# Optimization experiments

Hardware: AMD Instinct MI355X
Metric: run time of the kernel (lower is better)

The kernel has to match this reference:

```python
import jax, jax.numpy as jnp
import numpy as np

STRIDES = (8, 16, 32, 64, 128)
LEVEL_HW = ((128, 160), (64, 80), (32, 40), (16, 20), (8, 10))
IMG_H, IMG_W = 1024, 1280
B, NUM_CLASSES = 16, 20
SCORE_THR, IOU_THR, MAX_DET = 0.05, 0.6, 1000


def _coords_all():
    # coords_fmap2orig for every level, concatenated -> [N, 2] (x, y)
    cs = []
    for (h, w), s in zip(LEVEL_HW, STRIDES):
        sx = jnp.arange(w, dtype=jnp.float32) * s + s // 2
        sy = jnp.arange(h, dtype=jnp.float32) * s + s // 2
        yy, xx = jnp.meshgrid(sy, sx, indexing='ij')
        cs.append(jnp.stack([xx.reshape(-1), yy.reshape(-1)], -1))
    return jnp.concatenate(cs, 0)


def _reshape_cat(levels):
    # list of [B,C,h,w] -> [B, sum(h*w), C]
    return jnp.concatenate(
        [p.transpose(0, 2, 3, 1).reshape(p.shape[0], -1, p.shape[1]) for p in levels], 1)


def _decode(cls_l, cnt_l, reg_l, coords):
    cls = jax.nn.sigmoid(_reshape_cat(cls_l))           # [B,N,C]
    cnt = jax.nn.sigmoid(_reshape_cat(cnt_l))[..., 0]   # [B,N]
    reg = _reshape_cat(reg_l)                           # [B,N,4] ltrb
    scores = jnp.sqrt(jnp.max(cls, -1) * cnt)           # add_centerness + sqrt
    classes = jnp.argmax(cls, -1) + 1
    boxes = jnp.concatenate([coords[None] - reg[..., :2], coords[None] + reg[..., 2:]], -1)
    return scores, classes, boxes


def _nms_keep(boxes, scores, classes, valid):
    # masked greedy per-class NMS on fixed size M; returns keep mask [M]
    boxes = jax.lax.stop_gradient(boxes)
    scores = jax.lax.stop_gradient(scores)
    maxc = jnp.max(jnp.where(valid[:, None], boxes, 0.0))
    b = boxes + (classes.astype(boxes.dtype) * (maxc + 1.0))[:, None]  # class offsets
    order = jnp.argsort(-jnp.where(valid, scores, -jnp.inf))
    b = b[order]
    v = valid[order]
    x1, y1, x2, y2 = b[:, 0], b[:, 1], b[:, 2], b[:, 3]
    areas = (x2 - x1 + 1.0) * (y2 - y1 + 1.0)
    iw = jnp.clip(jnp.minimum(x2[:, None], x2[None, :]) - jnp.maximum(x1[:, None], x1[None, :]) + 1.0, 0.0)
    ih = jnp.clip(jnp.minimum(y2[:, None], y2[None, :]) - jnp.maximum(y1[:, None], y1[None, :]) + 1.0, 0.0)
    inter = iw * ih
    iou = inter / (areas[:, None] + areas[None, :] - inter)
    M = boxes.shape[0]

    def body(i, carry):
        keep, sup = carry
        k = v[i] & (~sup[i])
        keep = keep.at[i].set(k)
        sup = sup | (k & (iou[i] > IOU_THR))
        return keep, sup

    keep_s, _ = jax.lax.fori_loop(0, M, body, (jnp.zeros(M, bool), jnp.zeros(M, bool)))
    return jnp.zeros(M, bool).at[order].set(keep_s)


def _forward(args):
    cls_r, cnt_r, reg_r = args[0:5], args[5:10], args[10:15]
    cls_i, cnt_i, reg_i = args[15:20], args[20:25], args[25:30]
    coords = _coords_all()
    s_r, c_r, b_r = _decode(cls_r, cnt_r, reg_r, coords)
    s_i, c_i, b_i = _decode(cls_i, cnt_i, reg_i, coords)
    scores = jnp.concatenate([s_r, s_i], 1)   # [B, 2N]
    classes = jnp.concatenate([c_r, c_i], 1)
    boxes = jnp.concatenate([b_r, b_i], 1)
    top_s, top_i = jax.lax.top_k(scores, MAX_DET)
    top_c = jnp.take_along_axis(classes, top_i, 1)
    top_b = jnp.take_along_axis(boxes, top_i[..., None], 1)
    valid = top_s >= SCORE_THR
    keep = jax.vmap(_nms_keep)(top_b, top_s, top_c, valid)
    # ClipBoxes: clamp to image bounds
    top_b = jnp.maximum(top_b, 0.0)
    xs = jnp.minimum(top_b[..., 0::2], IMG_W - 1.0)
    ys = jnp.minimum(top_b[..., 1::2], IMG_H - 1.0)
    top_b = jnp.stack([xs[..., 0], ys[..., 0], xs[..., 1], ys[..., 1]], -1)
    kf = keep.astype(top_s.dtype)
    return top_s * kf, top_c * keep, top_b * kf[..., None], keep


def setup_inputs() -> dict:
    key = jax.random.key(0)
    chans = {'cls': NUM_CLASSES, 'cnt': 1, 'reg': 4}
    inp = {}
    i = 0
    for mod in ('r', 'i'):
        for kind in ('cls', 'cnt', 'reg'):
            for l, (h, w) in enumerate(LEVEL_HW):
                k = jax.random.fold_in(key, i); i += 1
                inp[f'{kind}_{mod}_{l}'] = jax.random.normal(k, (B, chans[kind], h, w), jnp.float32)
    return inp


def reference(cls_r_0, cls_r_1, cls_r_2, cls_r_3, cls_r_4,
              cnt_r_0, cnt_r_1, cnt_r_2, cnt_r_3, cnt_r_4,
              reg_r_0, reg_r_1, reg_r_2, reg_r_3, reg_r_4,
              cls_i_0, cls_i_1, cls_i_2, cls_i_3, cls_i_4,
              cnt_i_0, cnt_i_1, cnt_i_2, cnt_i_3, cnt_i_4,
              reg_i_0, reg_i_1, reg_i_2, reg_i_3, reg_i_4):
    args = [cls_r_0, cls_r_1, cls_r_2, cls_r_3, cls_r_4,
            cnt_r_0, cnt_r_1, cnt_r_2, cnt_r_3, cnt_r_4,
            reg_r_0, reg_r_1, reg_r_2, reg_r_3, reg_r_4,
            cls_i_0, cls_i_1, cls_i_2, cls_i_3, cls_i_4,
            cnt_i_0, cnt_i_1, cnt_i_2, cnt_i_3, cnt_i_4,
            reg_i_0, reg_i_1, reg_i_2, reg_i_3, reg_i_4]
    return _forward(args)
```

## Files before the change

### kernel.cpp

```cpp
#include <hip/hip_runtime.h>
#include <hip/hip_bf16.h>

typedef unsigned long long u64;
typedef unsigned int u32;

#define NTOT    54560
#define NMOD    27280
#define BATCH   16
#define KPAD    1024
#define MAXD    1000
#define NBIN    16384
#define CANDCAP 6144
#define NLDSPOS 25600

struct Ptrs { const float* p[30]; };

constexpr size_t SZ_KEY   = (size_t)BATCH * NTOT * 8;
constexpr size_t SZ_TOPK  = (size_t)BATCH * KPAD * 8;
constexpr size_t SZ_TRAW  = (size_t)BATCH * KPAD * 16;
constexpr size_t SZ_T1    = (size_t)BATCH * KPAD * 4;
constexpr size_t SZ_MAXC  = (size_t)BATCH * 32 * 4;
constexpr size_t SZ_VALID = (size_t)BATCH * 32 * 4;
constexpr size_t SZ_MASK  = (size_t)BATCH * KPAD * 32 * 4;

constexpr size_t OFF_KEY    = 0;
constexpr size_t OFF_TOPK   = OFF_KEY   + SZ_KEY;
constexpr size_t OFF_TRAW   = OFF_TOPK  + SZ_TOPK;
constexpr size_t OFF_TSCORE = OFF_TRAW  + SZ_TRAW;
constexpr size_t OFF_TCLSF  = OFF_TSCORE+ SZ_T1;
constexpr size_t OFF_MAXC   = OFF_TCLSF + SZ_T1;
constexpr size_t OFF_VALID  = OFF_MAXC  + SZ_MAXC;
constexpr size_t OFF_MASK   = OFF_VALID + SZ_VALID;

__device__ inline void level_of(int nm, int& l, int& pos, int& w, int& s, int& hw) {
    if (nm < 20480)      { l = 0; pos = nm;         w = 160; s = 8;   hw = 20480; }
    else if (nm < 25600) { l = 1; pos = nm - 20480; w = 80;  s = 16;  hw = 5120; }
    else if (nm < 26880) { l = 2; pos = nm - 25600; w = 40;  s = 32;  hw = 1280; }
    else if (nm < 27200) { l = 3; pos = nm - 26880; w = 20;  s = 64;  hw = 320; }
    else                 { l = 4; pos = nm - 27200; w = 10;  s = 128; hw = 80; }
}

__device__ inline float sigm(float x) { return 1.0f / (1.0f + expf(-x)); }

__device__ inline void ld_lds16(const float* g, float* l) {
    __builtin_amdgcn_global_load_lds(
        (const __attribute__((address_space(1))) void*)g,
        (__attribute__((address_space(3))) void*)l, 16, 0, 0);
}

__global__ __launch_bounds__(256)
void decode_lds_kernel(Ptrs ptrs, u64* __restrict__ keyAll) {
    __shared__ float lds[21 * 1024];
    int cc = blockIdx.x;
    int b = blockIdx.y;
    int mod = cc / 25, c = cc % 25;
    int l     = (c < 20) ? 0 : 1;
    int hw    = (c < 20) ? 20480 : 5120;
    int pos0  = (c < 20) ? c * 1024 : (c - 20) * 1024;
    int nmb   = (l == 0) ? pos0 : 20480 + pos0;
    const float* clsP = ptrs.p[mod * 15 + l];
    const float* cntP = ptrs.p[mod * 15 + 5 + l];
    int wave = threadIdx.x >> 6, lane = threadIdx.x & 63;

    const float* cbase = clsP + (size_t)b * 20 * hw + pos0 + wave * 256 + lane * 4;
    float* dbase = lds + wave * 256;
    #pragma unroll
    for (int ch = 0; ch < 20; ++ch)
        ld_lds16(cbase + (size_t)ch * hw, dbase + ch * 1024);
    ld_lds16(cntP + (size_t)b * hw + pos0 + wave * 256 + lane * 4, dbase + 20 * 1024);
    __syncthreads();

    int t = threadIdx.x;
    const float4* l4 = (const float4*)lds;
    float4 mx = l4[t];
    #pragma unroll
    for (int ch = 1; ch < 20; ++ch) {
        float4 v = l4[ch * 256 + t];
        mx.x = fmaxf(mx.x, v.x); mx.y = fmaxf(mx.y, v.y);
        mx.z = fmaxf(mx.z, v.z); mx.w = fmaxf(mx.w, v.w);
    }
    float4 cv = l4[20 * 256 + t];

    int n = mod * NMOD + nmb + t * 4;
    u32 s0 = __float_as_uint(sqrtf(__fmul_rn(sigm(mx.x), sigm(cv.x))));
    u32 s1 = __float_as_uint(sqrtf(__fmul_rn(sigm(mx.y), sigm(cv.y))));
    u32 s2 = __float_as_uint(sqrtf(__fmul_rn(sigm(mx.z), sigm(cv.z))));
    u32 s3 = __float_as_uint(sqrtf(__fmul_rn(sigm(mx.w), sigm(cv.w))));
    ulonglong2* ka2 = (ulonglong2*)(keyAll + (size_t)b * NTOT + n);
    ulonglong2 k01, k23;
    k01.x = ((u64)s0 << 16) | (u64)(65535 - n);
    k01.y = ((u64)s1 << 16) | (u64)(65535 - (n + 1));
    k23.x = ((u64)s2 << 16) | (u64)(65535 - (n + 2));
    k23.y = ((u64)s3 << 16) | (u64)(65535 - (n + 3));
    ka2[0] = k01; ka2[1] = k23;
}

__global__ __launch_bounds__(256)
void decode_tail_kernel(Ptrs ptrs, u64* __restrict__ keyAll) {
    int t = blockIdx.x * 256 + threadIdx.x;
    int b = blockIdx.y;
    if (t >= 3360) return;
    int mod = t / 1680;
    int tm = t % 1680;
    int q = t & 3;
    int nm = 25600 + (tm & ~3);
    int l, pos, w, s, hw;
    level_of(nm, l, pos, w, s, hw);
    (void)w; (void)s;
    const float* clsP = ptrs.p[mod * 15 + l];
    const float* cntP = ptrs.p[mod * 15 + 5 + l];
    const float4* cb = (const float4*)(clsP + (size_t)b * 20 * hw + pos);
    int hw4 = hw >> 2;
    int c0 = q * 5;
    float4 v[5];
    #pragma unroll
    for (int c = 0; c < 5; ++c) v[c] = cb[(size_t)(c0 + c) * hw4];
    float4 cv = *(const float4*)(cntP + (size_t)b * hw + pos);

    float4 mx = v[0];
    #pragma unroll
    for (int c = 1; c < 5; ++c) {
        mx.x = fmaxf(mx.x, v[c].x); mx.y = fmaxf(mx.y, v[c].y);
        mx.z = fmaxf(mx.z, v[c].z); mx.w = fmaxf(mx.w, v[c].w);
    }
    mx.x = fmaxf(mx.x, __shfl_xor(mx.x, 1));
    mx.y = fmaxf(mx.y, __shfl_xor(mx.y, 1));
    mx.z = fmaxf(mx.z, __shfl_xor(mx.z, 1));
    mx.w = fmaxf(mx.w, __shfl_xor(mx.w, 1));
    mx.x = fmaxf(mx.x, __shfl_xor(mx.x, 2));
    mx.y = fmaxf(mx.y, __shfl_xor(mx.y, 2));
    mx.z = fmaxf(mx.z, __shfl_xor(mx.z, 2));
    mx.w = fmaxf(mx.w, __shfl_xor(mx.w, 2));

    float ma = (q & 1) ? ((q & 2) ? mx.w : mx.y) : ((q & 2) ? mx.z : mx.x);
    float ca = (q & 1) ? ((q & 2) ? cv.w : cv.y) : ((q & 2) ? cv.z : cv.x);
    u32 sb = __float_as_uint(sqrtf(__fmul_rn(sigm(ma), sigm(ca))));
    int n = mod * NMOD + nm + q;
    keyAll[(size_t)b * NTOT + n] = ((u64)sb << 16) | (u64)(65535 - n);
}

__global__ __launch_bounds__(1024)
void select_kernel(const u64* __restrict__ keyAll, u64* __restrict__ topkey,
                   u32* __restrict__ maxcG) {
    int b = blockIdx.x, tid = threadIdx.x;
    int lane = tid & 63, wid = tid >> 6;
    __shared__ u32 shist[NBIN];
    __shared__ u32 warep[16];
    __shared__ int sB1;
    __shared__ u32 scnt;
    double* sd = (double*)shist;

    if (tid == 0) { maxcG[b * 32] = 0u; scnt = 0u; }
    #pragma unroll
    for (int j = 0; j < NBIN / 1024; ++j) shist[tid + j * 1024] = 0u;
    __syncthreads();

    const u64* keys = keyAll + (size_t)b * NTOT;
    const u64 SENT = ~0ull;
    for (int n0 = 0; n0 < NTOT; n0 += 8192) {
        u64 kk[8];
        #pragma unroll
        for (int r = 0; r < 8; ++r) {
            int idx = n0 + r * 1024 + tid;
            kk[r] = (idx < NTOT) ? keys[idx] : SENT;
        }
        #pragma unroll
        for (int r = 0; r < 8; ++r)
            if (kk[r] != SENT) atomicAdd(&shist[(u32)(kk[r] >> 32)], 1u);
    }
    __syncthreads();

    u32 loc[16]; u32 sum = 0;
    #pragma unroll
    for (int j = 0; j < 16; ++j) { loc[j] = shist[NBIN - 1 - (tid * 16 + j)]; sum += loc[j]; }
    u32 v = sum;
    #pragma unroll
    for (int off = 1; off < 64; off <<= 1) {
        u32 t2 = (u32)__shfl_up((int)v, off);
        if (lane >= off) v += t2;
    }
    if (lane == 63) warep[wid] = v;
    __syncthreads();
    if (tid < 16) {
        u32 p = warep[tid];
        #pragma unroll
        for (int off = 1; off < 16; off <<= 1) {
            u32 t2 = (u32)__shfl_up((int)p, off);
            if (tid >= off) p += t2;
        }
        warep[tid] = p;
    }
    __syncthreads();
    u32 incl = v + (wid ? warep[wid - 1] : 0u);
    u32 excl = incl - sum;
    if (excl < (u32)MAXD && incl >= (u32)MAXD) {
        u32 c = excl;
        #pragma unroll
        for (int j = 0; j < 16; ++j) {
            c += loc[j];
            if (c >= (u32)MAXD) { sB1 = NBIN - 1 - (tid * 16 + j); break; }
        }
    }
    __syncthreads();
    int B1 = sB1;

    for (int n0 = 0; n0 < NTOT; n0 += 8192) {
        u64 kk[8];
        #pragma unroll
        for (int r = 0; r < 8; ++r) {
            int idx = n0 + r * 1024 + tid;
            kk[r] = (idx < NTOT) ? keys[idx] : 0ull;
        }
        #pragma unroll
        for (int r = 0; r < 8; ++r) {
            if (kk[r] != 0ull && (int)(kk[r] >> 32) >= B1) {
                u32 p = atomicAdd(&scnt, 1u);
                if (p < CANDCAP - 2) sd[p] = (double)kk[r];
            }
        }
    }
    __syncthreads();
    int C = min((int)scnt, CANDCAP - 2);
    if (tid == 0) { sd[C] = -1.0; sd[C + 1] = -1.0; }
    __syncthreads();

    for (int i = tid; i < C; i += 1024) {
        double ki = sd[i];
        int rank = 0;
        const double2* sd2 = (const double2*)sd;
        int C2 = (C + 1) >> 1;
        for (int j = 0; j < C2; ++j) {
            double2 v2 = sd2[j];
            rank += (v2.x > ki) ? 1 : 0;
            rank += (v2.y > ki) ? 1 : 0;
        }
        if (rank < MAXD) topkey[(size_t)b * KPAD + rank] = (u64)ki;
    }
}

__global__ __launch_bounds__(128)
void gather_kernel(Ptrs ptrs, const u64* __restrict__ topkey,
                   float4* __restrict__ traw, float* __restrict__ tscore,
                   float* __restrict__ tclsf, u32* __restrict__ validwords,
                   u32* __restrict__ maxcG) {
    #pragma clang fp contract(off)
    int b = blockIdx.y;
    int tid = threadIdx.x;
    int half = tid & 1;
    int i = blockIdx.x * 64 + (tid >> 1);
    int active = (i < MAXD);

    float score = 0.f;
    float best = -1.0f; int bi = 0;
    float ra = 0.f, rb2 = 0.f;
    int pos = 0, w = 1, s = 0;
    if (active) {
        u64 key = topkey[(size_t)b * KPAD + i];
        int n = 65535 - (int)(key & 0xFFFFull);
        score = __uint_as_float((u32)(key >> 16));
        int mod = (n >= NMOD) ? 1 : 0;
        int nm = n - mod * NMOD;
        int l, hw;
        level_of(nm, l, pos, w, s, hw);
        const float* clsP = ptrs.p[mod * 15 + l];
        const float* regP = ptrs.p[mod * 15 + 10 + l];
        const float* cbp = clsP + (size_t)b * 20 * hw + pos;
        const float* rbp = regP + (size_t)b * 4 * hw + pos;
        float cl[10];
        int c0 = half * 10;
        #pragma unroll
        for (int c = 0; c < 10; ++c) cl[c] = cbp[(size_t)(c0 + c) * hw];
        ra  = rbp[(size_t)(half * 2) * hw];
        rb2 = rbp[(size_t)(half * 2 + 1) * hw];
        #pragma unroll
        for (int c = 0; c < 10; ++c) {
            float p = sigm(cl[c]);
            if (p > best) { best = p; bi = c0 + c; }
        }
    }
    float po  = __shfl_xor(best, 1);
    int   bio = __shfl_xor(bi, 1);
    float rao = __shfl_xor(ra, 1);
    float rbo = __shfl_xor(rb2, 1);
    if (half == 0) { if (po > best)  { best = po; bi = bio; } }
    else           { if (po >= best) { best = po; bi = bio; } }
    float clsf = active ? (float)(bi + 1) : 0.f;
    float r0 = half ? rao : ra,  r1 = half ? rbo : rb2;
    float r2 = half ? ra  : rao, r3 = half ? rb2 : rbo;

    float4 bx = make_float4(0.f, 0.f, 0.f, 0.f);
    if (active) {
        int xi = pos % w, yi = pos / w;
        float cx = (float)(xi * s + (s >> 1));
        float cy = (float)(yi * s + (s >> 1));
        bx.x = cx - r0; bx.y = cy - r1; bx.z = cx + r2; bx.w = cy + r3;
    }
    int valid = active && (score >= 0.05f) && (half == 0);
    float contrib = valid ? fmaxf(0.0f, fmaxf(fmaxf(bx.x, bx.y), fmaxf(bx.z, bx.w))) : 0.0f;
    float red = contrib;
    #pragma unroll
    for (int off = 32; off > 0; off >>= 1) red = fmaxf(red, __shfl_down(red, off));
    if ((tid & 63) == 0) atomicMax(&maxcG[b * 32], __float_as_uint(red));
    u64 ball = __ballot(valid != 0);
    if ((tid & 63) == 0) {
        u32 word = 0;
        for (int j = 0; j < 32; ++j) word |= (u32)((ball >> (2 * j)) & 1ull) << j;
        validwords[b * 32 + blockIdx.x * 2 + (tid >> 6)] = word;
    }
    if (half == 0) {
        size_t oo = (size_t)b * KPAD + i;
        traw[oo] = bx; tscore[oo] = score; tclsf[oo] = clsf;
    }
}

#define SW(t) ((((t) & 31) << 3) | ((t) >> 5))
__global__ __launch_bounds__(64)
void mask_kernel(const float4* __restrict__ traw, const float* __restrict__ tclsf,
                 const u32* __restrict__ maxcG, u32* __restrict__ maskG) {
    #pragma clang fp contract(off)
    int u = blockIdx.x, b = blockIdx.y, tid = threadIdx.x;
    int g, wg;
    if (u < 128)      { g = u >> 2;                 wg = u & 3; }
    else if (u < 224) { int i2 = u - 128; g = 32 + i2 / 3;      wg = 1 + i2 % 3; }
    else if (u < 288) { int i2 = u - 224; g = 64 + (i2 >> 1);   wg = 2 + (i2 & 1); }
    else              { g = 96 + (u - 288);         wg = 3; }
    int i0 = g * 8, j0 = wg * 256;
    float m1 = __uint_as_float(maxcG[b * 32]) + 1.0f;

    __shared__ float cx1[256], cy1[256], cx2[256], cy2[256], ca[256];
    for (int t = tid; t < 256; t += 64) {
        float4 f = traw[(size_t)b * KPAD + j0 + t];
        float o = __fmul_rn(tclsf[(size_t)b * KPAD + j0 + t], m1);
        float ox1 = __fadd_rn(f.x, o), oy1 = __fadd_rn(f.y, o);
        float ox2 = __fadd_rn(f.z, o), oy2 = __fadd_rn(f.w, o);
        float dw = ox2 - ox1 + 1.0f;
        float dh = oy2 - oy1 + 1.0f;
        int ts = SW(t);
        cx1[ts] = ox1; cy1[ts] = oy1; cx2[ts] = ox2; cy2[ts] = oy2;
        ca[ts] = __fmul_rn(dw, dh);
    }
    __syncthreads();

    int ir = tid >> 3, wr = tid & 7;
    int i = i0 + ir;
    float4 fi = traw[(size_t)b * KPAD + i];
    float oi = __fmul_rn(tclsf[(size_t)b * KPAD + i], m1);
    float ix1 = __fadd_rn(fi.x, oi), iy1 = __fadd_rn(fi.y, oi);
    float ix2 = __fadd_rn(fi.z, oi), iy2 = __fadd_rn(fi.w, oi);
    float dwi = ix2 - ix1 + 1.0f, dhi = iy2 - iy1 + 1.0f;
    float ai = __fmul_rn(dwi, dhi);
    u32 bits = 0;
    int jb = wr * 32;
    for (int jj = 0; jj < 32; ++jj) {
        int js = SW(jb + jj);
        float iw = fminf(ix2, cx2[js]) - fmaxf(ix1, cx1[js]) + 1.0f;
        iw = fmaxf(iw, 0.0f);
        float ih = fminf(iy2, cy2[js]) - fmaxf(iy1, cy1[js]) + 1.0f;
        ih = fmaxf(ih, 0.0f);
        float inter = iw * ih;
        float denom = (ai + ca[js]) - inter;
        float iou = inter / denom;
        bits |= (iou > 0.6f) ? (1u << jj) : 0u;
    }
    maskG[((size_t)b * KPAD + i) * 32 + wg * 8 + wr] = bits;
}

__global__ __launch_bounds__(512)
void scan_out_kernel(const u32* __restrict__ maskG, const u32* __restrict__ validbits,
                     const float4* __restrict__ traw, const float* __restrict__ tscore,
                     const float* __restrict__ tclsf, float* __restrict__ out) {
    __shared__ u32 sm[KPAD * 32];
    __shared__ u32 keeps[32];
    int b = blockIdx.x, tid = threadIdx.x;

    const uint4* s4 = (const uint4*)(maskG + (size_t)b * KPAD * 32);
    uint4* d4 = (uint4*)sm;
    #pragma unroll
    for (int r = 0; r < 16; ++r) d4[tid + r * 512] = s4[tid + r * 512];
    __syncthreads();

    if (tid < 64) {
        int lane = tid, lw = lane & 31;
        u32 vreg = (lane < 32) ? validbits[b * 32 + lane] : 0u;
        u32 removed = 0u, keepw = 0u;
        u32 mA[8], mB[8];
        #pragma unroll
        for (int d = 0; d < 8; ++d) {
            mA[d] = sm[d * 32 + lw];
            mB[d] = sm[(d + 8) * 32 + lw];
        }
        auto step8 = [&](int base, u32* ms) {
            #pragma unroll
            for (int d = 0; d < 8; ++d) {
                int i = base + d;
                int wi = i >> 5, bi2 = i & 31;
                u32 rw = (u32)__builtin_amdgcn_readlane((int)removed, wi);
                u32 vw = (u32)__builtin_amdgcn_readlane((int)vreg, wi);
                u32 k = ((vw >> bi2) & 1u) & (~(rw >> bi2) & 1u);
                if (k) removed |= ms[d];
                if (lane == wi) keepw |= (k << bi2);
                ms[d] = sm[(i + 16) * 32 + lw];
            }
        };
        for (int t = 0; t < 62; ++t) { step8(t * 16, mA); step8(t * 16 + 8, mB); }
        step8(992, mA);
        if (lane < 32) keeps[lane] = keepw;
    }
    __syncthreads();

    const int BQ = BATCH * MAXD;
    for (int s2 = tid; s2 < MAXD; s2 += 512) {
        u32 kf = (keeps[s2 >> 5] >> (s2 & 31)) & 1u;
        size_t oo = (size_t)b * KPAD + s2;
        float score = tscore[oo];
        float clsf = tclsf[oo];
        float4 bx = traw[oo];
        float x1 = fminf(fmaxf(bx.x, 0.f), 1279.f);
        float y1 = fminf(fmaxf(bx.y, 0.f), 1023.f);
        float x2 = fminf(fmaxf(bx.z, 0.f), 1279.f);
        float y2 = fminf(fmaxf(bx.w, 0.f), 1023.f);
        int base = b * MAXD + s2;
        out[base] = kf ? score : 0.0f;
        out[BQ + base] = kf ? clsf : 0.0f;
        float* ob = out + 2 * BQ + (size_t)base * 4;
        ob[0] = kf ? x1 : 0.f; ob[1] = kf ? y1 : 0.f;
        ob[2] = kf ? x2 : 0.f; ob[3] = kf ? y2 : 0.f;
        out[6 * BQ + base] = kf ? 1.0f : 0.0f;
    }
}

extern "C" void kernel_launch(void* const* d_in, const int* in_sizes, int n_in,
                              void* d_out, int out_size, void* d_ws, size_t ws_size,
                              hipStream_t stream) {
    Ptrs ptrs;
    for (int i = 0; i < 30; ++i) ptrs.p[i] = (const float*)d_in[i];

    char* ws = (char*)d_ws;
    u64*    keyAll    = (u64*)   (ws + OFF_KEY);
    u64*    topkey    = (u64*)   (ws + OFF_TOPK);
    float4* traw      = (float4*)(ws + OFF_TRAW);
    float*  tscore    = (float*) (ws + OFF_TSCORE);
    float*  tclsf     = (float*) (ws + OFF_TCLSF);
    u32*    maxcG     = (u32*)   (ws + OFF_MAXC);
    u32*    validbits = (u32*)   (ws + OFF_VALID);
    u32*    maskG     = (u32*)   (ws + OFF_MASK);
    float*  out       = (float*)d_out;

    decode_lds_kernel<<<dim3(50, BATCH), 256, 0, stream>>>(ptrs, keyAll);
    decode_tail_kernel<<<dim3(14, BATCH), 256, 0, stream>>>(ptrs, keyAll);
    select_kernel<<<BATCH, 1024, 0, stream>>>(keyAll, topkey, maxcG);
    gather_kernel<<<dim3(16, BATCH), 128, 0, stream>>>(ptrs, topkey, traw, tscore, tclsf,
                                                       validbits, maxcG);
    mask_kernel<<<dim3(320, BATCH), 64, 0, stream>>>(traw, tclsf, maxcG, maskG);
    scan_out_kernel<<<BATCH, 512, 0, stream>>>(maskG, validbits, traw, tscore, tclsf, out);
}
```

Measured before the change: 277.6 us.

## Fuse decode kernels, bucket-based top-k ranking, and larger mask tiles

Merges the two decode kernels into one launch with smaller 128-thread blocks. In the select kernel, it replaces the O(C^2) all-pairs rank count over doubles with a counting-sort scatter into histogram-bin buckets, followed by ranking within each bin. It also stages the top-k in LDS before writing it out. The mask kernel is retiled to 256-thread blocks covering 32 rows each, so fewer blocks are launched. The main risk is ranking cost when one bin holds many candidates, and the candidate count being capped at CAND.

Result: faster. 253.2 us (-8.8%).

```diff
diff --git a/kernel.cpp b/kernel.cpp
--- a/kernel.cpp
+++ b/kernel.cpp
@@ -10,8 +10,7 @@
 #define KPAD    1024
 #define MAXD    1000
 #define NBIN    16384
-#define CANDCAP 6144
-#define NLDSPOS 25600
+#define CAND    6144
 
 struct Ptrs { const float* p[30]; };
 
@@ -48,15 +47,57 @@
         (__attribute__((address_space(3))) void*)l, 16, 0, 0);
 }
 
-__global__ __launch_bounds__(256)
-void decode_lds_kernel(Ptrs ptrs, u64* __restrict__ keyAll) {
-    __shared__ float lds[21 * 1024];
+__global__ __launch_bounds__(128)
+void decode_kernel(Ptrs ptrs, u64* __restrict__ keyAll) {
+    __shared__ float lds[21 * 512];
     int cc = blockIdx.x;
     int b = blockIdx.y;
-    int mod = cc / 25, c = cc % 25;
-    int l     = (c < 20) ? 0 : 1;
-    int hw    = (c < 20) ? 20480 : 5120;
-    int pos0  = (c < 20) ? c * 1024 : (c - 20) * 1024;
+
+    if (cc >= 100) {
+        int t = (cc - 100) * 128 + threadIdx.x;
+        if (t >= 3360) return;
+        int mod = t / 1680;
+        int tm = t % 1680;
+        int q = t & 3;
+        int nm = 25600 + (tm & ~3);
+        int l, pos, w, s, hw;
+        level_of(nm, l, pos, w, s, hw);
+        (void)w; (void)s;
+        const float* clsP = ptrs.p[mod * 15 + l];
+        const float* cntP = ptrs.p[mod * 15 + 5 + l];
+        const float4* cb = (const float4*)(clsP + (size_t)b * 20 * hw + pos);
+        int hw4 = hw >> 2;
+        int c0 = q * 5;
+        float4 v[5];
+        #pragma unroll
+        for (int c = 0; c < 5; ++c) v[c] = cb[(size_t)(c0 + c) * hw4];
+        float4 cv = *(const float4*)(cntP + (size_t)b * hw + pos);
+        float4 mx = v[0];
+        #pragma unroll
+        for (int c = 1; c < 5; ++c) {
+            mx.x = fmaxf(mx.x, v[c].x); mx.y = fmaxf(mx.y, v[c].y);
+            mx.z = fmaxf(mx.z, v[c].z); mx.w = fmaxf(mx.w, v[c].w);
+        }
+        mx.x = fmaxf(mx.x, __shfl_xor(mx.x, 1));
+        mx.y = fmaxf(mx.y, __shfl_xor(mx.y, 1));
+        mx.z = fmaxf(mx.z, __shfl_xor(mx.z, 1));
+        mx.w = fmaxf(mx.w, __shfl_xor(mx.w, 1));
+        mx.x = fmaxf(mx.x, __shfl_xor(mx.x, 2));
+        mx.y = fmaxf(mx.y, __shfl_xor(mx.y, 2));
+        mx.z = fmaxf(mx.z, __shfl_xor(mx.z, 2));
+        mx.w = fmaxf(mx.w, __shfl_xor(mx.w, 2));
+        float ma = (q & 1) ? ((q & 2) ? mx.w : mx.y) : ((q & 2) ? mx.z : mx.x);
+        float ca = (q & 1) ? ((q & 2) ? cv.w : cv.y) : ((q & 2) ? cv.z : cv.x);
+        u32 sb = __float_as_uint(sqrtf(__fmul_rn(sigm(ma), sigm(ca))));
+        int n = mod * NMOD + nm + q;
+        keyAll[(size_t)b * NTOT + n] = ((u64)sb << 16) | (u64)(65535 - n);
+        return;
+    }
+
+    int mod = cc / 50, c = cc % 50;
+    int l     = (c < 40) ? 0 : 1;
+    int hw    = (c < 40) ? 20480 : 5120;
+    int pos0  = (c < 40) ? c * 512 : (c - 40) * 512;
     int nmb   = (l == 0) ? pos0 : 20480 + pos0;
     const float* clsP = ptrs.p[mod * 15 + l];
     const float* cntP = ptrs.p[mod * 15 + 5 + l];
@@ -66,8 +107,8 @@
     float* dbase = lds + wave * 256;
     #pragma unroll
     for (int ch = 0; ch < 20; ++ch)
-        ld_lds16(cbase + (size_t)ch * hw, dbase + ch * 1024);
-    ld_lds16(cntP + (size_t)b * hw + pos0 + wave * 256 + lane * 4, dbase + 20 * 1024);
+        ld_lds16(cbase + (size_t)ch * hw, dbase + ch * 512);
+    ld_lds16(cntP + (size_t)b * hw + pos0 + wave * 256 + lane * 4, dbase + 20 * 512);
     __syncthreads();
 
     int t = threadIdx.x;
@@ -75,11 +116,11 @@
     float4 mx = l4[t];
     #pragma unroll
     for (int ch = 1; ch < 20; ++ch) {
-        float4 v = l4[ch * 256 + t];
+        float4 v = l4[ch * 128 + t];
         mx.x = fmaxf(mx.x, v.x); mx.y = fmaxf(mx.y, v.y);
         mx.z = fmaxf(mx.z, v.z); mx.w = fmaxf(mx.w, v.w);
     }
-    float4 cv = l4[20 * 256 + t];
+    float4 cv = l4[20 * 128 + t];
 
     int n = mod * NMOD + nmb + t * 4;
     u32 s0 = __float_as_uint(sqrtf(__fmul_rn(sigm(mx.x), sigm(cv.x))));
@@ -95,62 +136,18 @@
     ka2[0] = k01; ka2[1] = k23;
 }
 
-__global__ __launch_bounds__(256)
-void decode_tail_kernel(Ptrs ptrs, u64* __restrict__ keyAll) {
-    int t = blockIdx.x * 256 + threadIdx.x;
-    int b = blockIdx.y;
-    if (t >= 3360) return;
-    int mod = t / 1680;
-    int tm = t % 1680;
-    int q = t & 3;
-    int nm = 25600 + (tm & ~3);
-    int l, pos, w, s, hw;
-    level_of(nm, l, pos, w, s, hw);
-    (void)w; (void)s;
-    const float* clsP = ptrs.p[mod * 15 + l];
-    const float* cntP = ptrs.p[mod * 15 + 5 + l];
-    const float4* cb = (const float4*)(clsP + (size_t)b * 20 * hw + pos);
-    int hw4 = hw >> 2;
-    int c0 = q * 5;
-    float4 v[5];
-    #pragma unroll
-    for (int c = 0; c < 5; ++c) v[c] = cb[(size_t)(c0 + c) * hw4];
-    float4 cv = *(const float4*)(cntP + (size_t)b * hw + pos);
-
-    float4 mx = v[0];
-    #pragma unroll
-    for (int c = 1; c < 5; ++c) {
-        mx.x = fmaxf(mx.x, v[c].x); mx.y = fmaxf(mx.y, v[c].y);
-        mx.z = fmaxf(mx.z, v[c].z); mx.w = fmaxf(mx.w, v[c].w);
-    }
-    mx.x = fmaxf(mx.x, __shfl_xor(mx.x, 1));
-    mx.y = fmaxf(mx.y, __shfl_xor(mx.y, 1));
-    mx.z = fmaxf(mx.z, __shfl_xor(mx.z, 1));
-    mx.w = fmaxf(mx.w, __shfl_xor(mx.w, 1));
-    mx.x = fmaxf(mx.x, __shfl_xor(mx.x, 2));
-    mx.y = fmaxf(mx.y, __shfl_xor(mx.y, 2));
-    mx.z = fmaxf(mx.z, __shfl_xor(mx.z, 2));
-    mx.w = fmaxf(mx.w, __shfl_xor(mx.w, 2));
-
-    float ma = (q & 1) ? ((q & 2) ? mx.w : mx.y) : ((q & 2) ? mx.z : mx.x);
-    float ca = (q & 1) ? ((q & 2) ? cv.w : cv.y) : ((q & 2) ? cv.z : cv.x);
-    u32 sb = __float_as_uint(sqrtf(__fmul_rn(sigm(ma), sigm(ca))));
-    int n = mod * NMOD + nm + q;
-    keyAll[(size_t)b * NTOT + n] = ((u64)sb << 16) | (u64)(65535 - n);
-}
-
 __global__ __launch_bounds__(1024)
 void select_kernel(const u64* __restrict__ keyAll, u64* __restrict__ topkey,
                    u32* __restrict__ maxcG) {
     int b = blockIdx.x, tid = threadIdx.x;
     int lane = tid & 63, wid = tid >> 6;
     __shared__ u32 shist[NBIN];
+    __shared__ u64 scand[CAND];
+    __shared__ u64 stopk[KPAD];
     __shared__ u32 warep[16];
     __shared__ int sB1;
-    __shared__ u32 scnt;
-    double* sd = (double*)shist;
-
-    if (tid == 0) { maxcG[b * 32] = 0u; scnt = 0u; }
+
+    if (tid == 0) maxcG[b * 32] = 0u;
     #pragma unroll
     for (int j = 0; j < NBIN / 1024; ++j) shist[tid + j * 1024] = 0u;
     __syncthreads();
@@ -201,6 +198,13 @@
             if (c >= (u32)MAXD) { sB1 = NBIN - 1 - (tid * 16 + j); break; }
         }
     }
+    u32 run = excl;
+    #pragma unroll
+    for (int j = 0; j < 16; ++j) {
+        int bin = NBIN - 1 - (tid * 16 + j);
+        shist[bin] = run;
+        run += loc[j];
+    }
     __syncthreads();
     int B1 = sB1;
 
@@ -214,28 +218,25 @@
         #pragma unroll
         for (int r = 0; r < 8; ++r) {
             if (kk[r] != 0ull && (int)(kk[r] >> 32) >= B1) {
-                u32 p = atomicAdd(&scnt, 1u);
-                if (p < CANDCAP - 2) sd[p] = (double)kk[r];
+                u32 p = atomicAdd(&shist[(u32)(kk[r] >> 32)], 1u);
+                if (p < CAND) scand[p] = kk[r];
             }
         }
     }
     __syncthreads();
-    int C = min((int)scnt, CANDCAP - 2);
-    if (tid == 0) { sd[C] = -1.0; sd[C + 1] = -1.0; }
-    __syncthreads();
-
-    for (int i = tid; i < C; i += 1024) {
-        double ki = sd[i];
-        int rank = 0;
-        const double2* sd2 = (const double2*)sd;
-        int C2 = (C + 1) >> 1;
-        for (int j = 0; j < C2; ++j) {
-            double2 v2 = sd2[j];
-            rank += (v2.x > ki) ? 1 : 0;
-            rank += (v2.y > ki) ? 1 : 0;
-        }
-        if (rank < MAXD) topkey[(size_t)b * KPAD + rank] = (u64)ki;
-    }
+    int Ctot = min((int)shist[B1], CAND);
+
+    for (int i = tid; i < Ctot; i += 1024) {
+        u64 ki = scand[i];
+        int bin = (int)(ki >> 32);
+        int st = (int)shist[bin + 1];
+        int en = min((int)shist[bin], Ctot);
+        int pos = st;
+        for (int j = st; j < en; ++j) pos += (scand[j] > ki) ? 1 : 0;
+        if (pos < MAXD) stopk[pos] = ki;
+    }
+    __syncthreads();
+    if (tid < MAXD) topkey[(size_t)b * KPAD + tid] = stopk[tid];
 }
 
 __global__ __launch_bounds__(128)
@@ -314,21 +315,22 @@
 }
 
 #define SW(t) ((((t) & 31) << 3) | ((t) >> 5))
-__global__ __launch_bounds__(64)
+__global__ __launch_bounds__(256)
 void mask_kernel(const float4* __restrict__ traw, const float* __restrict__ tclsf,
                  const u32* __restrict__ maxcG, u32* __restrict__ maskG) {
     #pragma clang fp contract(off)
     int u = blockIdx.x, b = blockIdx.y, tid = threadIdx.x;
     int g, wg;
-    if (u < 128)      { g = u >> 2;                 wg = u & 3; }
-    else if (u < 224) { int i2 = u - 128; g = 32 + i2 / 3;      wg = 1 + i2 % 3; }
-    else if (u < 288) { int i2 = u - 224; g = 64 + (i2 >> 1);   wg = 2 + (i2 & 1); }
-    else              { g = 96 + (u - 288);         wg = 3; }
-    int i0 = g * 8, j0 = wg * 256;
+    if (u < 32)      { g = u >> 2;              wg = u & 3; }
+    else if (u < 56) { int d = u - 32; g = 8  + d / 3;        wg = 1 + d % 3; }
+    else if (u < 72) { int d = u - 56; g = 16 + (d >> 1);     wg = 2 + (d & 1); }
+    else             { g = 24 + (u - 72);       wg = 3; }
+    int i0 = g * 32, j0 = wg * 256;
     float m1 = __uint_as_float(maxcG[b * 32]) + 1.0f;
 
     __shared__ float cx1[256], cy1[256], cx2[256], cy2[256], ca[256];
-    for (int t = tid; t < 256; t += 64) {
+    {
+        int t = tid;
         float4 f = traw[(size_t)b * KPAD + j0 + t];
         float o = __fmul_rn(tclsf[(size_t)b * KPAD + j0 + t], m1);
         float ox1 = __fadd_rn(f.x, o), oy1 = __fadd_rn(f.y, o);
@@ -446,11 +448,10 @@
     u32*    maskG     = (u32*)   (ws + OFF_MASK);
     float*  out       = (float*)d_out;
 
-    decode_lds_kernel<<<dim3(50, BATCH), 256, 0, stream>>>(ptrs, keyAll);
-    decode_tail_kernel<<<dim3(14, BATCH), 256, 0, stream>>>(ptrs, keyAll);
+    decode_kernel<<<dim3(127, BATCH), 128, 0, stream>>>(ptrs, keyAll);
     select_kernel<<<BATCH, 1024, 0, stream>>>(keyAll, topkey, maxcG);
     gather_kernel<<<dim3(16, BATCH), 128, 0, stream>>>(ptrs, topkey, traw, tscore, tclsf,
                                                        validbits, maxcG);
-    mask_kernel<<<dim3(320, BATCH), 64, 0, stream>>>(traw, tclsf, maxcG, maskG);
+    mask_kernel<<<dim3(80, BATCH), 256, 0, stream>>>(traw, tclsf, maxcG, maskG);
     scan_out_kernel<<<BATCH, 512, 0, stream>>>(maskG, validbits, traw, tscore, tclsf, out);
 }
```
